# Kernel optimization log

Hardware: AMD Instinct MI355X
Metric: run time of the kernel (lower is better)

The kernel has to match this reference:

```python
import jax, jax.numpy as jnp
import numpy as np

B, K, D = 4096, 100, 64          # batch, multi_factor*top_k, emb_dim
NU, NI = 100000, 50000           # n_users, n_items
MLP_DIMS = [2 * K, K, K // 2, 25, 12, 1]  # 200,100,50,25,12,1


def setup_inputs() -> dict:
    key = jax.random.key(0)
    ks = jax.random.split(key, 30)
    inp = {
        "user_idxs": jax.random.randint(ks[0], (B,), 0, NU),
        "item_idxs": jax.random.randint(ks[1], (B,), 0, NI),
        "user_idx_tensor": jax.random.randint(ks[2], (NU, K), 0, NU),
        "item_idx_tensor": jax.random.randint(ks[3], (NI, K), 0, NI),
        "user_scr_tensor": jax.random.uniform(ks[4], (NU, K), dtype=jnp.float32),
        "item_scr_tensor": jax.random.uniform(ks[5], (NI, K), dtype=jnp.float32),
        "user_emb": jax.random.normal(ks[6], (NU, D), dtype=jnp.float32),
        "item_emb": jax.random.normal(ks[7], (NI, D), dtype=jnp.float32),
    }
    i = 8
    for net in ("n1", "n2"):
        for li, (a, b) in enumerate(zip(MLP_DIMS[:-1], MLP_DIMS[1:]), 1):
            lim = 1.0 / np.sqrt(a)
            inp[f"{net}_w{li}"] = jax.random.uniform(ks[i], (a, b), minval=-lim, maxval=lim, dtype=jnp.float32); i += 1
            inp[f"{net}_b{li}"] = jax.random.uniform(ks[i], (b,), minval=-lim, maxval=lim, dtype=jnp.float32); i += 1
    return inp


def _mlp(x, ws, bs):
    for w, b in zip(ws[:-1], bs[:-1]):
        x = jax.nn.relu(x @ w + b)
    return x @ ws[-1] + bs[-1]


def reference(user_idxs, item_idxs, user_idx_tensor, item_idx_tensor,
              user_scr_tensor, item_scr_tensor, user_emb, item_emb,
              n1_w1, n1_b1, n1_w2, n1_b2, n1_w3, n1_b3, n1_w4, n1_b4, n1_w5, n1_b5,
              n2_w1, n2_b1, n2_w2, n2_b2, n2_w3, n2_b3, n2_w4, n2_b4, n2_w5, n2_b5):
    # neighbor gather: [B,K,D] embeddings and [B,K] scores
    u_e = user_emb[user_idx_tensor[user_idxs]]
    u_s = user_scr_tensor[user_idxs]
    i_e = item_emb[item_idx_tensor[item_idxs]]
    i_s = item_scr_tensor[item_idxs]
    # torch bmm(emb [B,K,D], score[:,None,:].repeat(1,D,1) [B,D,K]) -> [B,K,K];
    # since the repeated score matrix has identical rows, result = emb.sum(-1) (x) score
    su = u_e.sum(-1)[:, :, None] * u_s[:, None, :]  # [B,K,K]
    si = i_e.sum(-1)[:, :, None] * i_s[:, None, :]  # [B,K,K]
    # cat(dim=1).permute(0,2,1) == cat of transposes along last dim
    x1 = jnp.concatenate([su.transpose(0, 2, 1), si.transpose(0, 2, 1)], axis=2)  # [B,K,2K]
    x2 = jnp.concatenate([su, si], axis=2)                                        # [B,K,2K]
    ws1 = [n1_w1, n1_w2, n1_w3, n1_w4, n1_w5]; bs1 = [n1_b1, n1_b2, n1_b3, n1_b4, n1_b5]
    ws2 = [n2_w1, n2_w2, n2_w3, n2_w4, n2_w5]; bs2 = [n2_b1, n2_b2, n2_b3, n2_b4, n2_b5]
    c1 = _mlp(x1, ws1, bs1)[..., 0]  # [B,K]
    c2 = _mlp(x2, ws2, bs2)[..., 0]  # [B,K]
    return jax.nn.sigmoid(jnp.mean(c1 + c2, axis=1))  # [B]
```

## Files before the change

### kernel.cpp

```cpp
#include <hip/hip_runtime.h>
#include <math.h>

#define KDIM 100
#define DDIM 64

typedef __bf16 bf16x8 __attribute__((ext_vector_type(8)));
typedef float  f32x4  __attribute__((ext_vector_type(4)));
typedef float  f32x2  __attribute__((ext_vector_type(2)));
typedef unsigned int u32;
typedef u32 u32x2 __attribute__((ext_vector_type(2)));

struct Weights {
  const float *w1, *b1, *w2, *b2, *w3, *b3, *w4, *b4, *w5, *b5;
};

__device__ __forceinline__ f32x2 vmax2(f32x2 a, f32x2 b) {
#if __has_builtin(__builtin_elementwise_max)
  return __builtin_elementwise_max(a, b);
#else
  return (f32x2){fmaxf(a[0], b[0]), fmaxf(a[1], b[1])};
#endif
}

constexpr int L_VEC  = 0;
constexpr int L_PA   = 400;
constexpr int L_TAIL = 912;
constexpr int L_C    = 1424;
constexpr int SM_F   = 1680;
constexpr int H2T_BYTE = SM_F * 4;
constexpr int H3T_BYTE = H2T_BYTE + 8 * 2048;
constexpr int SM_BYTES = H3T_BYTE + 8 * 1024;

__global__ void prep_kernel(const float* __restrict__ user_emb,
                            const float* __restrict__ item_emb,
                            float* __restrict__ u_rowsum,
                            float* __restrict__ i_rowsum,
                            int NU, int NI, Weights N1, Weights N2,
                            __bf16* __restrict__ wfrag, float* __restrict__ tail) {
  const int tid  = threadIdx.x;
  const int lane = tid & 63;
  const int g = lane >> 4, c16 = lane & 15;
  const int gw = (blockIdx.x * blockDim.x + tid) >> 6;

  if (gw < 42) {
    const int net = gw / 21, f = gw % 21;
    const Weights W = net ? N2 : N1;
    bf16x8 v;
    if (f < 16) {
      const int mt = f >> 2, ks = f & 3;
      #pragma unroll
      for (int i = 0; i < 8; ++i) {
        const int k = 32 * ks + 8 * g + i, m = 16 * mt + c16;
        v[i] = (__bf16)((k < 100 && m < 50) ? W.w2[k * 50 + m] : 0.f);
      }
    } else if (f < 20) {
      const int mt = (f - 16) >> 1, ks = (f - 16) & 1;
      #pragma unroll
      for (int i = 0; i < 8; ++i) {
        const int k = 32 * ks + 8 * g + i, m = 16 * mt + c16;
        v[i] = (__bf16)((k < 50 && m < 25) ? W.w3[k * 25 + m] : 0.f);
      }
    } else {
      #pragma unroll
      for (int i = 0; i < 8; ++i) {
        const int k = 8 * g + i, m = c16;
        v[i] = (__bf16)((k < 25 && m < 12) ? W.w4[k * 12 + m] : 0.f);
      }
    }
    *(bf16x8*)(wfrag + (size_t)gw * 512 + lane * 8) = v;
  }

  if (blockIdx.x == 0) {
    for (int e = tid; e < 512; e += 256) {
      float v;
      if (e < 256)      { const int j = e & 127; const Weights W = (e & 128) ? N2 : N1; v = (j < 100) ? W.b1[j] : 0.f; }
      else if (e < 384) { const int t = e - 256; const int j = t & 63; const Weights W = (t & 64) ? N2 : N1; v = (j < 50) ? W.b2[j] : 0.f; }
      else if (e < 448) { const int t = e - 384; const int j = t & 31; const Weights W = (t & 32) ? N2 : N1; v = (j < 25) ? W.b3[j] : 0.f; }
      else if (e < 480) { const int t = e - 448; const int j = t & 15; const Weights W = (t & 16) ? N2 : N1; v = (j < 12) ? W.b4[j] : 0.f; }
      else              { const int t = e - 480; const int j = t & 15; const Weights W = (t & 16) ? N2 : N1; v = (j < 12) ? W.w5[j] : 0.f; }
      tail[e] = v;
    }
  }

  const int NR = NU + NI;
  const int chunk = lane & 15, lrow = lane >> 4;
  const int nwave = (gridDim.x * blockDim.x) >> 6;
  for (int base = gw * 4; base < NR; base += nwave * 4) {
    const int r = base + lrow;
    float s = 0.f;
    if (r < NR) {
      const float* src = (r < NU) ? (user_emb + (size_t)r * DDIM)
                                  : (item_emb + (size_t)(r - NU) * DDIM);
      const float4 v4 = ((const float4*)src)[chunk];
      s = v4.x + v4.y + v4.z + v4.w;
    }
    s += __shfl_xor(s, 1); s += __shfl_xor(s, 2);
    s += __shfl_xor(s, 4); s += __shfl_xor(s, 8);
    if (chunk == 0 && r < NR) {
      if (r < NU) u_rowsum[r] = s; else i_rowsum[r - NU] = s;
    }
  }
}

__global__ void __launch_bounds__(256) proj_kernel(
    const int* __restrict__ user_idxs, const int* __restrict__ item_idxs,
    const int* __restrict__ uidx_t, const int* __restrict__ iidx_t,
    const float* __restrict__ uscr, const float* __restrict__ iscr,
    const float* __restrict__ u_rowsum, const float* __restrict__ i_rowsum,
    const float* __restrict__ n1w1, const float* __restrict__ n2w1,
    float* __restrict__ VG, float* __restrict__ PAG, int B)
{
  __shared__ float VT[100][20];
  __shared__ float W1S[50][128];
  __shared__ int sidx[16];
  const int tid = threadIdx.x;
  const int sel = blockIdx.x & 3;
  const int b0  = (blockIdx.x >> 2) * 16;

  if (tid < 16) {
    const int b = b0 + tid;
    const int bb = (b < B) ? b : (B - 1);
    sidx[tid] = (sel & 1) ? item_idxs[bb] : user_idxs[bb];
  }
  __syncthreads();

  {
    const int bl = tid >> 4, strip = tid & 15;
    const size_t row = (size_t)sidx[bl] * KDIM;
    if (sel < 2) {
      const int* it = (sel == 0) ? uidx_t : iidx_t;
      const float* rs = (sel == 0) ? u_rowsum : i_rowsum;
      int idxs[7];
      #pragma unroll
      for (int i = 0; i < 7; ++i) {
        const int k = strip + 16 * i;
        idxs[i] = (k < KDIM) ? it[row + k] : 0;
      }
      #pragma unroll
      for (int i = 0; i < 7; ++i) {
        const int k = strip + 16 * i;
        if (k < KDIM) VT[k][bl] = rs[idxs[i]];
      }
    } else {
      const float* sc = (sel == 2) ? uscr : iscr;
      #pragma unroll
      for (int i = 0; i < 7; ++i) {
        const int k = strip + 16 * i;
        if (k < KDIM) VT[k][bl] = sc[row + k];
      }
    }
  }

  const float* w1 = (sel < 2) ? n1w1 : n2w1;
  const int rb = (sel & 1) * KDIM;
  const int jg = tid & 31, bg = tid >> 5;
  float acc[2][4];
  #pragma unroll
  for (int bi = 0; bi < 2; ++bi)
    #pragma unroll
    for (int ji = 0; ji < 4; ++ji) acc[bi][ji] = 0.f;

  for (int kh = 0; kh < 2; ++kh) {
    __syncthreads();
    for (int e = tid; e < 1600; e += 256) {
      const int k = e >> 5, s = e & 31;
      float4 v;
      if (s < 25) v = ((const float4*)(w1 + (size_t)(rb + kh * 50 + k) * KDIM))[s];
      else        v = make_float4(0.f, 0.f, 0.f, 0.f);
      *(float4*)&W1S[k][4 * s] = v;
    }
    __syncthreads();
    #pragma unroll 2
    for (int k = 0; k < 50; ++k) {
      const f32x2 v = *(const f32x2*)&VT[kh * 50 + k][2 * bg];
      const float4 w = *(const float4*)&W1S[k][4 * jg];
      const float ww[4] = {w.x, w.y, w.z, w.w};
      #pragma unroll
      for (int ji = 0; ji < 4; ++ji) {
        acc[0][ji] = fmaf(v[0], ww[ji], acc[0][ji]);
        acc[1][ji] = fmaf(v[1], ww[ji], acc[1][ji]);
      }
    }
  }

  #pragma unroll
  for (int bi = 0; bi < 2; ++bi) {
    const int b = b0 + 2 * bg + bi;
    if (b < B) {
      float4 o = make_float4(acc[bi][0], acc[bi][1], acc[bi][2], acc[bi][3]);
      *(float4*)(PAG + ((size_t)sel * B + b) * 128 + 4 * jg) = o;
    }
  }
  {
    const int bl = tid >> 4, strip = tid & 15;
    const int b = b0 + bl;
    if (b < B) {
      float* dst = VG + ((size_t)sel * B + b) * KDIM;
      #pragma unroll
      for (int i = 0; i < 7; ++i) {
        const int k = strip + 16 * i;
        if (k < KDIM) dst[k] = VT[k][bl];
      }
    }
  }
}

__global__ void __launch_bounds__(512, 4) mlp_kernel(
    const float* __restrict__ VG, const float* __restrict__ PAG,
    const float* __restrict__ tail,
    const float* __restrict__ n1b5, const float* __restrict__ n2b5,
    const __bf16* __restrict__ wfrag, float* __restrict__ out, int B)
{
  __shared__ __align__(16) char smem[SM_BYTES];
  float* sm = (float*)smem;
  const int tid  = threadIdx.x;
  const int lane = tid & 63;
  const int wv   = tid >> 6;
  const int g    = lane >> 4;
  const int c16  = lane & 15;
  const int b    = blockIdx.x;
  const f32x2 Z2 = {0.f, 0.f};

  if (tid < 128) {
    const int sel = tid >> 5, s = tid & 31;
    *(float4*)&sm[L_PA + sel * 128 + 4 * s] =
        *(const float4*)(PAG + ((size_t)sel * B + b) * 128 + 4 * s);
  } else if (tid < 256) {
    const int t = tid - 128;
    *(float4*)&sm[L_TAIL + 4 * t] = *(const float4*)(tail + 4 * t);
  } else if (tid < 456) {
    const int e = tid - 256;
    const int sel = e / 50, r = e % 50;
    *(f32x2*)&sm[L_VEC + sel * 100 + 2 * r] =
        *(const f32x2*)(VG + ((size_t)sel * B + b) * KDIM + 2 * r);
  }
  __syncthreads();

  const int net = wv >> 2;
  const int q   = wv & 3;
  const int r0  = 25 * q;
  const int vA  = net ? (L_VEC + 0)   : (L_VEC + 200);
  const int vB  = net ? (L_VEC + 100) : (L_VEC + 300);
  const int pAo = L_PA + net * 256;
  const int pBo = pAo + 128;
  const char* wfb = (const char*)wfrag + net * 21 * 1024;
  char* h2t = smem + H2T_BYTE + wv * 2048;
  char* h3t = smem + H3T_BYTE + wv * 1024;
  const float b5v = net ? n2b5[0] : n1b5[0];
  const int t7 = c16 & 7, t3 = c16 & 3;

  float sAr[2], sBr[2];
  #pragma unroll
  for (int c = 0; c < 2; ++c) {
    const int row = r0 + 16 * c + c16;
    const int rr = row < KDIM ? row : (KDIM - 1);
    sAr[c] = sm[vA + rr]; sBr[c] = sm[vB + rr];
  }

  f32x4 acc2[2][4];
  #pragma unroll
  for (int c = 0; c < 2; ++c)
    #pragma unroll
    for (int mt = 0; mt < 4; ++mt) acc2[c][mt] = (f32x4){0.f, 0.f, 0.f, 0.f};

  #pragma unroll
  for (int ks = 0; ks < 4; ++ks) {
    const int jb = 32 * ks + 8 * g;
    const f32x2* pa2 = (const f32x2*)&sm[pAo + jb];
    const f32x2* pb2 = (const f32x2*)&sm[pBo + jb];
    const f32x2* b12 = (const f32x2*)&sm[L_TAIL + net * 128 + jb];
    f32x2 paf[4], pbf[4], b1f[4];
    #pragma unroll
    for (int i = 0; i < 4; ++i) { paf[i] = pa2[i]; pbf[i] = pb2[i]; b1f[i] = b12[i]; }
    bf16x8 hb[2];
    #pragma unroll
    for (int c = 0; c < 2; ++c) {
      const f32x2 sa = {sAr[c], sAr[c]}, sb = {sBr[c], sBr[c]};
      bf16x8 a;
      #pragma unroll
      for (int i2 = 0; i2 < 4; ++i2) {
        f32x2 t = sb * pbf[i2] + b1f[i2];
        t = sa * paf[i2] + t;
        t = vmax2(t, Z2);
        a[2 * i2]     = (__bf16)t[0];
        a[2 * i2 + 1] = (__bf16)t[1];
      }
      hb[c] = a;
    }
    __builtin_amdgcn_s_setprio(1);
    #pragma unroll
    for (int mt = 0; mt < 4; ++mt) {
      const bf16x8 a = *(const bf16x8*)(wfb + (mt * 4 + ks) * 1024 + lane * 16);
      acc2[0][mt] = __builtin_amdgcn_mfma_f32_16x16x32_bf16(a, hb[0], acc2[0][mt], 0, 0, 0);
      acc2[1][mt] = __builtin_amdgcn_mfma_f32_16x16x32_bf16(a, hb[1], acc2[1][mt], 0, 0, 0);
    }
    __builtin_amdgcn_s_setprio(0);
  }

  #pragma unroll
  for (int c = 0; c < 2; ++c) {
    #pragma unroll
    for (int mt = 0; mt < 4; ++mt) {
      const f32x2* b2p = (const f32x2*)&sm[L_TAIL + 256 + net * 64 + 16 * mt + 4 * g];
      const f32x4 x = acc2[c][mt];
      const f32x2 lo = vmax2((f32x2){x[0], x[1]} + b2p[0], Z2);
      const f32x2 hi = vmax2((f32x2){x[2], x[3]} + b2p[1], Z2);
      union { __bf16 e[4]; u32x2 w; } o;
      o.e[0] = (__bf16)lo[0]; o.e[1] = (__bf16)lo[1];
      o.e[2] = (__bf16)hi[0]; o.e[3] = (__bf16)hi[1];
      const int S = (2 * mt + (g >> 1)) ^ t7;
      *(u32x2*)(h2t + c16 * 128 + S * 16 + (g & 1) * 8) = o.w;
    }

    f32x4 acc3[2];
    #pragma unroll
    for (int mt = 0; mt < 2; ++mt) acc3[mt] = (f32x4){0.f, 0.f, 0.f, 0.f};
    #pragma unroll
    for (int ks = 0; ks < 2; ++ks) {
      const int S = (4 * ks + g) ^ t7;
      const bf16x8 hbf = *(const bf16x8*)(h2t + c16 * 128 + S * 16);
      __builtin_amdgcn_s_setprio(1);
      #pragma unroll
      for (int mt = 0; mt < 2; ++mt) {
        const bf16x8 a = *(const bf16x8*)(wfb + (16 + mt * 2 + ks) * 1024 + lane * 16);
        acc3[mt] = __builtin_amdgcn_mfma_f32_16x16x32_bf16(a, hbf, acc3[mt], 0, 0, 0);
      }
      __builtin_amdgcn_s_setprio(0);
    }
    #pragma unroll
    for (int mt = 0; mt < 2; ++mt) {
      const f32x2* b3p = (const f32x2*)&sm[L_TAIL + 384 + net * 32 + 16 * mt + 4 * g];
      const f32x4 x = acc3[mt];
      const f32x2 lo = vmax2((f32x2){x[0], x[1]} + b3p[0], Z2);
      const f32x2 hi = vmax2((f32x2){x[2], x[3]} + b3p[1], Z2);
      union { __bf16 e[4]; u32x2 w; } o;
      o.e[0] = (__bf16)lo[0]; o.e[1] = (__bf16)lo[1];
      o.e[2] = (__bf16)hi[0]; o.e[3] = (__bf16)hi[1];
      const int S = (2 * mt + (g >> 1)) ^ t3;
      *(u32x2*)(h3t + c16 * 64 + S * 16 + (g & 1) * 8) = o.w;
    }

    {
      const int S = g ^ t3;
      const bf16x8 hbf = *(const bf16x8*)(h3t + c16 * 64 + S * 16);
      const bf16x8 a = *(const bf16x8*)(wfb + 20 * 1024 + lane * 16);
      const f32x4 z = {0.f, 0.f, 0.f, 0.f};
      __builtin_amdgcn_s_setprio(1);
      const f32x4 acc4 = __builtin_amdgcn_mfma_f32_16x16x32_bf16(a, hbf, z, 0, 0, 0);
      __builtin_amdgcn_s_setprio(0);
      const f32x2* b4p = (const f32x2*)&sm[L_TAIL + 448 + net * 16 + 4 * g];
      const f32x2* w5p = (const f32x2*)&sm[L_TAIL + 480 + net * 16 + 4 * g];
      const f32x2 lo = vmax2((f32x2){acc4[0], acc4[1]} + b4p[0], Z2);
      const f32x2 hi = vmax2((f32x2){acc4[2], acc4[3]} + b4p[1], Z2);
      float v = lo[0] * w5p[0][0] + lo[1] * w5p[0][1]
              + hi[0] * w5p[1][0] + hi[1] * w5p[1][1];
      v += __shfl_xor(v, 16); v += __shfl_xor(v, 32);
      const int lr = 16 * c + c16;
      if (g == 0 && lr < 25)
        sm[L_C + net * 128 + r0 + lr] = v + b5v;
    }
  }
  __syncthreads();

  float v = 0.f;
  if (tid < KDIM) v = sm[L_C + tid] + sm[L_C + 128 + tid];
  if (tid < 128) {
    #pragma unroll
    for (int d = 1; d < 64; d <<= 1) v += __shfl_xor(v, d);
    if ((tid & 63) == 0) sm[tid >> 6] = v;
  }
  __syncthreads();
  if (tid == 0) out[b] = 1.f / (1.f + expf(-0.01f * (sm[0] + sm[1])));
}

extern "C" void kernel_launch(void* const* d_in, const int* in_sizes, int n_in,
                              void* d_out, int out_size, void* d_ws, size_t ws_size,
                              hipStream_t stream) {
  const int*   user_idxs = (const int*)d_in[0];
  const int*   item_idxs = (const int*)d_in[1];
  const int*   uidx_t    = (const int*)d_in[2];
  const int*   iidx_t    = (const int*)d_in[3];
  const float* uscr      = (const float*)d_in[4];
  const float* iscr      = (const float*)d_in[5];
  const float* uemb      = (const float*)d_in[6];
  const float* iemb      = (const float*)d_in[7];

  const int B  = in_sizes[0];
  const int NU = in_sizes[6] / DDIM;
  const int NI = in_sizes[7] / DDIM;

  Weights N1 { (const float*)d_in[8],  (const float*)d_in[9],
               (const float*)d_in[10], (const float*)d_in[11],
               (const float*)d_in[12], (const float*)d_in[13],
               (const float*)d_in[14], (const float*)d_in[15],
               (const float*)d_in[16], (const float*)d_in[17] };
  Weights N2 { (const float*)d_in[18], (const float*)d_in[19],
               (const float*)d_in[20], (const float*)d_in[21],
               (const float*)d_in[22], (const float*)d_in[23],
               (const float*)d_in[24], (const float*)d_in[25],
               (const float*)d_in[26], (const float*)d_in[27] };

  char* ws = (char*)d_ws;
  float* u_rowsum = (float*)ws;
  float* i_rowsum = u_rowsum + NU;
  size_t off = (((size_t)(NU + NI) * 4 + 1023) & ~(size_t)1023);
  __bf16* wfrag = (__bf16*)(ws + off);
  float*  tail  = (float*)(wfrag + (size_t)42 * 512);
  off += (((size_t)42 * 512 * 2 + 512 * 4 + 1023) & ~(size_t)1023);
  float* VG  = (float*)(ws + off);
  off += (size_t)4 * B * KDIM * 4;
  float* PAG = (float*)(ws + off);

  float* out = (float*)d_out;

  prep_kernel<<<1024, 256, 0, stream>>>(uemb, iemb, u_rowsum, i_rowsum, NU, NI, N1, N2, wfrag, tail);
  const int nbt = (B + 15) / 16;
  proj_kernel<<<nbt * 4, 256, 0, stream>>>(user_idxs, item_idxs, uidx_t, iidx_t,
                                           uscr, iscr, u_rowsum, i_rowsum,
                                           N1.w1, N2.w1, VG, PAG, B);
  mlp_kernel<<<B, 512, 0, stream>>>(VG, PAG, tail, N1.b5, N2.b5, wfrag, out, B);
}
```

Measured before the change: 79.63 us.

## Process two batch rows per MLP block to reuse loaded weight fragments

Each mlp_kernel block now handles two batch elements instead of one, loading the layer-1 bf16 weight fragments once per k-step and feeding them to MFMAs for both rows. The grid is halved, and shared memory and the per-wave scratch buffers are doubled. Launch bounds drop from 4 to 2 blocks per CU, trading occupancy and more registers for fewer weight loads and less per-block setup overhead.

After: 86.18 us. 8.2% more time.

```diff
diff --git a/kernel.cpp b/kernel.cpp
--- a/kernel.cpp
+++ b/kernel.cpp
@@ -23,13 +23,13 @@
 }
 
 constexpr int L_VEC  = 0;
-constexpr int L_PA   = 400;
-constexpr int L_TAIL = 912;
-constexpr int L_C    = 1424;
-constexpr int SM_F   = 1680;
+constexpr int L_PA   = 800;
+constexpr int L_TAIL = 1824;
+constexpr int L_C    = 2336;
+constexpr int SM_F   = 2848;
 constexpr int H2T_BYTE = SM_F * 4;
-constexpr int H3T_BYTE = H2T_BYTE + 8 * 2048;
-constexpr int SM_BYTES = H3T_BYTE + 8 * 1024;
+constexpr int H3T_BYTE = H2T_BYTE + 16 * 2048;
+constexpr int SM_BYTES = H3T_BYTE + 16 * 1024;
 
 __global__ void prep_kernel(const float* __restrict__ user_emb,
                             const float* __restrict__ item_emb,
@@ -205,7 +205,7 @@
   }
 }
 
-__global__ void __launch_bounds__(512, 4) mlp_kernel(
+__global__ void __launch_bounds__(512, 2) mlp_kernel(
     const float* __restrict__ VG, const float* __restrict__ PAG,
     const float* __restrict__ tail,
     const float* __restrict__ n1b5, const float* __restrict__ n2b5,
@@ -218,20 +218,25 @@
   const int wv   = tid >> 6;
   const int g    = lane >> 4;
   const int c16  = lane & 15;
-  const int b    = blockIdx.x;
+  const int b0   = blockIdx.x * 2;
+  const int b1   = b0 + 1;
+  const int bb1  = (b1 < B) ? b1 : (B - 1);
   const f32x2 Z2 = {0.f, 0.f};
 
-  if (tid < 128) {
-    const int sel = tid >> 5, s = tid & 31;
-    *(float4*)&sm[L_PA + sel * 128 + 4 * s] =
+  if (tid < 256) {
+    const int bat = tid >> 7, sel = (tid >> 5) & 3, s = tid & 31;
+    const int b = bat ? bb1 : b0;
+    *(float4*)&sm[L_PA + bat * 512 + sel * 128 + 4 * s] =
         *(const float4*)(PAG + ((size_t)sel * B + b) * 128 + 4 * s);
-  } else if (tid < 256) {
-    const int t = tid - 128;
+  } else if (tid < 384) {
+    const int t = tid - 256;
     *(float4*)&sm[L_TAIL + 4 * t] = *(const float4*)(tail + 4 * t);
-  } else if (tid < 456) {
-    const int e = tid - 256;
-    const int sel = e / 50, r = e % 50;
-    *(f32x2*)&sm[L_VEC + sel * 100 + 2 * r] =
+  }
+  if (tid < 400) {
+    const int bat = tid / 200, rem = tid % 200;
+    const int sel = rem / 50, r = rem % 50;
+    const int b = bat ? bb1 : b0;
+    *(f32x2*)&sm[L_VEC + bat * 400 + sel * 100 + 2 * r] =
         *(const f32x2*)(VG + ((size_t)sel * B + b) * KDIM + 2 * r);
   }
   __syncthreads();
@@ -239,115 +244,137 @@
   const int net = wv >> 2;
   const int q   = wv & 3;
   const int r0  = 25 * q;
-  const int vA  = net ? (L_VEC + 0)   : (L_VEC + 200);
-  const int vB  = net ? (L_VEC + 100) : (L_VEC + 300);
-  const int pAo = L_PA + net * 256;
-  const int pBo = pAo + 128;
   const char* wfb = (const char*)wfrag + net * 21 * 1024;
-  char* h2t = smem + H2T_BYTE + wv * 2048;
-  char* h3t = smem + H3T_BYTE + wv * 1024;
   const float b5v = net ? n2b5[0] : n1b5[0];
   const int t7 = c16 & 7, t3 = c16 & 3;
 
-  float sAr[2], sBr[2];
-  #pragma unroll
-  for (int c = 0; c < 2; ++c) {
-    const int row = r0 + 16 * c + c16;
-    const int rr = row < KDIM ? row : (KDIM - 1);
-    sAr[c] = sm[vA + rr]; sBr[c] = sm[vB + rr];
-  }
-
-  f32x4 acc2[2][4];
-  #pragma unroll
-  for (int c = 0; c < 2; ++c)
-    #pragma unroll
-    for (int mt = 0; mt < 4; ++mt) acc2[c][mt] = (f32x4){0.f, 0.f, 0.f, 0.f};
+  float sAr[2][2], sBr[2][2];
+  #pragma unroll
+  for (int bat = 0; bat < 2; ++bat)
+    #pragma unroll
+    for (int c = 0; c < 2; ++c) {
+      const int row = r0 + 16 * c + c16;
+      const int rr = row < KDIM ? row : (KDIM - 1);
+      const int vA = L_VEC + bat * 400 + (net ? 0 : 200);
+      sAr[bat][c] = sm[vA + rr]; sBr[bat][c] = sm[vA + 100 + rr];
+    }
+
+  f32x4 acc2[2][2][4];
+  #pragma unroll
+  for (int bat = 0; bat < 2; ++bat)
+    #pragma unroll
+    for (int c = 0; c < 2; ++c)
+      #pragma unroll
+      for (int mt = 0; mt < 4; ++mt) acc2[bat][c][mt] = (f32x4){0.f, 0.f, 0.f, 0.f};
 
   #pragma unroll
   for (int ks = 0; ks < 4; ++ks) {
     const int jb = 32 * ks + 8 * g;
-    const f32x2* pa2 = (const f32x2*)&sm[pAo + jb];
-    const f32x2* pb2 = (const f32x2*)&sm[pBo + jb];
+    bf16x8 bw[4];
+    #pragma unroll
+    for (int mt = 0; mt < 4; ++mt)
+      bw[mt] = *(const bf16x8*)(wfb + (mt * 4 + ks) * 1024 + lane * 16);
     const f32x2* b12 = (const f32x2*)&sm[L_TAIL + net * 128 + jb];
-    f32x2 paf[4], pbf[4], b1f[4];
-    #pragma unroll
-    for (int i = 0; i < 4; ++i) { paf[i] = pa2[i]; pbf[i] = pb2[i]; b1f[i] = b12[i]; }
-    bf16x8 hb[2];
-    #pragma unroll
-    for (int c = 0; c < 2; ++c) {
-      const f32x2 sa = {sAr[c], sAr[c]}, sb = {sBr[c], sBr[c]};
-      bf16x8 a;
-      #pragma unroll
-      for (int i2 = 0; i2 < 4; ++i2) {
-        f32x2 t = sb * pbf[i2] + b1f[i2];
-        t = sa * paf[i2] + t;
-        t = vmax2(t, Z2);
-        a[2 * i2]     = (__bf16)t[0];
-        a[2 * i2 + 1] = (__bf16)t[1];
-      }
-      hb[c] = a;
+    f32x2 b1f[4];
+    #pragma unroll
+    for (int i = 0; i < 4; ++i) b1f[i] = b12[i];
+    bf16x8 hb[2][2];
+    #pragma unroll
+    for (int bat = 0; bat < 2; ++bat) {
+      const f32x2* pa2 = (const f32x2*)&sm[L_PA + bat * 512 + net * 256 + jb];
+      const f32x2* pb2 = (const f32x2*)&sm[L_PA + bat * 512 + net * 256 + 128 + jb];
+      f32x2 paf[4], pbf[4];
+      #pragma unroll
+      for (int i = 0; i < 4; ++i) { paf[i] = pa2[i]; pbf[i] = pb2[i]; }
+      #pragma unroll
+      for (int c = 0; c < 2; ++c) {
+        const f32x2 sa = {sAr[bat][c], sAr[bat][c]};
+        const f32x2 sb = {sBr[bat][c], sBr[bat][c]};
+        bf16x8 a;
+        #pragma unroll
+        for (int i2 = 0; i2 < 4; ++i2) {
+          f32x2 t = sb * pbf[i2] + b1f[i2];
+          t = sa * paf[i2] + t;
+          t = vmax2(t, Z2);
+          a[2 * i2]     = (__bf16)t[0];
+          a[2 * i2 + 1] = (__bf16)t[1];
+        }
+        hb[bat][c] = a;
+      }
     }
     __builtin_amdgcn_s_setprio(1);
     #pragma unroll
-    for (int mt = 0; mt < 4; ++mt) {
-      const bf16x8 a = *(const bf16x8*)(wfb + (mt * 4 + ks) * 1024 + lane * 16);
-      acc2[0][mt] = __builtin_amdgcn_mfma_f32_16x16x32_bf16(a, hb[0], acc2[0][mt], 0, 0, 0);
-      acc2[1][mt] = __builtin_amdgcn_mfma_f32_16x16x32_bf16(a, hb[1], acc2[1][mt], 0, 0, 0);
-    }
+    for (int mt = 0; mt < 4; ++mt)
+      #pragma unroll
+      for (int bat = 0; bat < 2; ++bat) {
+        acc2[bat][0][mt] = __builtin_amdgcn_mfma_f32_16x16x32_bf16(bw[mt], hb[bat][0], acc2[bat][0][mt], 0, 0, 0);
+        acc2[bat][1][mt] = __builtin_amdgcn_mfma_f32_16x16x32_bf16(bw[mt], hb[bat][1], acc2[bat][1][mt], 0, 0, 0);
+      }
     __builtin_amdgcn_s_setprio(0);
   }
 
   #pragma unroll
   for (int c = 0; c < 2; ++c) {
     #pragma unroll
-    for (int mt = 0; mt < 4; ++mt) {
-      const f32x2* b2p = (const f32x2*)&sm[L_TAIL + 256 + net * 64 + 16 * mt + 4 * g];
-      const f32x4 x = acc2[c][mt];
-      const f32x2 lo = vmax2((f32x2){x[0], x[1]} + b2p[0], Z2);
-      const f32x2 hi = vmax2((f32x2){x[2], x[3]} + b2p[1], Z2);
-      union { __bf16 e[4]; u32x2 w; } o;
-      o.e[0] = (__bf16)lo[0]; o.e[1] = (__bf16)lo[1];
-      o.e[2] = (__bf16)hi[0]; o.e[3] = (__bf16)hi[1];
-      const int S = (2 * mt + (g >> 1)) ^ t7;
-      *(u32x2*)(h2t + c16 * 128 + S * 16 + (g & 1) * 8) = o.w;
-    }
-
-    f32x4 acc3[2];
-    #pragma unroll
-    for (int mt = 0; mt < 2; ++mt) acc3[mt] = (f32x4){0.f, 0.f, 0.f, 0.f};
-    #pragma unroll
-    for (int ks = 0; ks < 2; ++ks) {
-      const int S = (4 * ks + g) ^ t7;
-      const bf16x8 hbf = *(const bf16x8*)(h2t + c16 * 128 + S * 16);
-      __builtin_amdgcn_s_setprio(1);
+    for (int bat = 0; bat < 2; ++bat) {
+      char* h2t = smem + H2T_BYTE + (wv * 2 + bat) * 2048;
+      #pragma unroll
+      for (int mt = 0; mt < 4; ++mt) {
+        const f32x2* b2p = (const f32x2*)&sm[L_TAIL + 256 + net * 64 + 16 * mt + 4 * g];
+        const f32x4 x = acc2[bat][c][mt];
+        const f32x2 lo = vmax2((f32x2){x[0], x[1]} + b2p[0], Z2);
+        const f32x2 hi = vmax2((f32x2){x[2], x[3]} + b2p[1], Z2);
+        union { __bf16 e[4]; u32x2 w; } o;
+        o.e[0] = (__bf16)lo[0]; o.e[1] = (__bf16)lo[1];
+        o.e[2] = (__bf16)hi[0]; o.e[3] = (__bf16)hi[1];
+        const int S = (2 * mt + (g >> 1)) ^ t7;
+        *(u32x2*)(h2t + c16 * 128 + S * 16 + (g & 1) * 8) = o.w;
+      }
+    }
+
+    f32x4 acc3[2][2];
+    #pragma unroll
+    for (int bat = 0; bat < 2; ++bat)
+      #pragma unroll
+      for (int mt = 0; mt < 2; ++mt) acc3[bat][mt] = (f32x4){0.f, 0.f, 0.f, 0.f};
+    #pragma unroll
+    for (int bat = 0; bat < 2; ++bat) {
+      char* h2t = smem + H2T_BYTE + (wv * 2 + bat) * 2048;
+      #pragma unroll
+      for (int ks = 0; ks < 2; ++ks) {
+        const int S = (4 * ks + g) ^ t7;
+        const bf16x8 hbf = *(const bf16x8*)(h2t + c16 * 128 + S * 16);
+        #pragma unroll
+        for (int mt = 0; mt < 2; ++mt) {
+          const bf16x8 a = *(const bf16x8*)(wfb + (16 + mt * 2 + ks) * 1024 + lane * 16);
+          acc3[bat][mt] = __builtin_amdgcn_mfma_f32_16x16x32_bf16(a, hbf, acc3[bat][mt], 0, 0, 0);
+        }
+      }
+    }
+    #pragma unroll
+    for (int bat = 0; bat < 2; ++bat) {
+      char* h3t = smem + H3T_BYTE + (wv * 2 + bat) * 1024;
       #pragma unroll
       for (int mt = 0; mt < 2; ++mt) {
-        const bf16x8 a = *(const bf16x8*)(wfb + (16 + mt * 2 + ks) * 1024 + lane * 16);
-        acc3[mt] = __builtin_amdgcn_mfma_f32_16x16x32_bf16(a, hbf, acc3[mt], 0, 0, 0);
-      }
-      __builtin_amdgcn_s_setprio(0);
-    }
-    #pragma unroll
-    for (int mt = 0; mt < 2; ++mt) {
-      const f32x2* b3p = (const f32x2*)&sm[L_TAIL + 384 + net * 32 + 16 * mt + 4 * g];
-      const f32x4 x = acc3[mt];
-      const f32x2 lo = vmax2((f32x2){x[0], x[1]} + b3p[0], Z2);
-      const f32x2 hi = vmax2((f32x2){x[2], x[3]} + b3p[1], Z2);
-      union { __bf16 e[4]; u32x2 w; } o;
-      o.e[0] = (__bf16)lo[0]; o.e[1] = (__bf16)lo[1];
-      o.e[2] = (__bf16)hi[0]; o.e[3] = (__bf16)hi[1];
-      const int S = (2 * mt + (g >> 1)) ^ t3;
-      *(u32x2*)(h3t + c16 * 64 + S * 16 + (g & 1) * 8) = o.w;
-    }
-
-    {
+        const f32x2* b3p = (const f32x2*)&sm[L_TAIL + 384 + net * 32 + 16 * mt + 4 * g];
+        const f32x4 x = acc3[bat][mt];
+        const f32x2 lo = vmax2((f32x2){x[0], x[1]} + b3p[0], Z2);
+        const f32x2 hi = vmax2((f32x2){x[2], x[3]} + b3p[1], Z2);
+        union { __bf16 e[4]; u32x2 w; } o;
+        o.e[0] = (__bf16)lo[0]; o.e[1] = (__bf16)lo[1];
+        o.e[2] = (__bf16)hi[0]; o.e[3] = (__bf16)hi[1];
+        const int S = (2 * mt + (g >> 1)) ^ t3;
+        *(u32x2*)(h3t + c16 * 64 + S * 16 + (g & 1) * 8) = o.w;
+      }
+    }
+    #pragma unroll
+    for (int bat = 0; bat < 2; ++bat) {
+      char* h3t = smem + H3T_BYTE + (wv * 2 + bat) * 1024;
       const int S = g ^ t3;
       const bf16x8 hbf = *(const bf16x8*)(h3t + c16 * 64 + S * 16);
       const bf16x8 a = *(const bf16x8*)(wfb + 20 * 1024 + lane * 16);
       const f32x4 z = {0.f, 0.f, 0.f, 0.f};
-      __builtin_amdgcn_s_setprio(1);
       const f32x4 acc4 = __builtin_amdgcn_mfma_f32_16x16x32_bf16(a, hbf, z, 0, 0, 0);
-      __builtin_amdgcn_s_setprio(0);
       const f32x2* b4p = (const f32x2*)&sm[L_TAIL + 448 + net * 16 + 4 * g];
       const f32x2* w5p = (const f32x2*)&sm[L_TAIL + 480 + net * 16 + 4 * g];
       const f32x2 lo = vmax2((f32x2){acc4[0], acc4[1]} + b4p[0], Z2);
@@ -357,20 +384,25 @@
       v += __shfl_xor(v, 16); v += __shfl_xor(v, 32);
       const int lr = 16 * c + c16;
       if (g == 0 && lr < 25)
-        sm[L_C + net * 128 + r0 + lr] = v + b5v;
+        sm[L_C + bat * 256 + net * 128 + r0 + lr] = v + b5v;
     }
   }
   __syncthreads();
 
-  float v = 0.f;
-  if (tid < KDIM) v = sm[L_C + tid] + sm[L_C + 128 + tid];
-  if (tid < 128) {
-    #pragma unroll
-    for (int d = 1; d < 64; d <<= 1) v += __shfl_xor(v, d);
-    if ((tid & 63) == 0) sm[tid >> 6] = v;
+  {
+    const int bat = (tid >= 256) ? 1 : 0;
+    const int lt = tid & 255;
+    if (lt < 128) {
+      float v = 0.f;
+      if (lt < KDIM) v = sm[L_C + bat * 256 + lt] + sm[L_C + bat * 256 + 128 + lt];
+      #pragma unroll
+      for (int d = 1; d < 64; d <<= 1) v += __shfl_xor(v, d);
+      if ((lt & 63) == 0) sm[bat * 2 + (lt >> 6)] = v;
+    }
   }
   __syncthreads();
-  if (tid == 0) out[b] = 1.f / (1.f + expf(-0.01f * (sm[0] + sm[1])));
+  if (tid == 0) out[b0] = 1.f / (1.f + expf(-0.01f * (sm[0] + sm[1])));
+  else if (tid == 1 && b1 < B) out[b1] = 1.f / (1.f + expf(-0.01f * (sm[2] + sm[3])));
 }
 
 extern "C" void kernel_launch(void* const* d_in, const int* in_sizes, int n_in,
@@ -418,5 +450,5 @@
   proj_kernel<<<nbt * 4, 256, 0, stream>>>(user_idxs, item_idxs, uidx_t, iidx_t,
                                            uscr, iscr, u_rowsum, i_rowsum,
                                            N1.w1, N2.w1, VG, PAG, B);
-  mlp_kernel<<<B, 512, 0, stream>>>(VG, PAG, tail, N1.b5, N2.b5, wfrag, out, B);
+  mlp_kernel<<<(B + 1) / 2, 512, 0, stream>>>(VG, PAG, tail, N1.b5, N2.b5, wfrag, out, B);
 }
```
